# Optimization experiments

Hardware: AMD Instinct MI355X
Metric: run time of the kernel (lower is better)

The kernel has to match this reference:

```python
import jax, jax.numpy as jnp
import numpy as np
from jax import lax

K = 31      # avg_pool kernel
PAD = 15    # avg_pool padding (count_include_pad=True, torch default)
EPS = 1e-07

def _box_avg(x):
    # avg_pool2d(kernel=31, stride=1, padding=15), divisor includes zero padding
    s = lax.reduce_window(x, 0.0, lax.add, (1, 1, K, K), (1, 1, 1, 1),
                          [(0, 0), (0, 0), (PAD, PAD), (PAD, PAD)])
    return s / (K * K)

def _bce_logits(x, t):
    # stable elementwise BCE-with-logits
    return jnp.maximum(x, 0.0) - x * t + jnp.log1p(jnp.exp(-jnp.abs(x)))

def setup_inputs() -> dict:
    key = jax.random.key(0)
    k1, k2 = jax.random.split(key)
    B, C, H, W = 32, 1, 384, 384
    inp = jax.random.normal(k1, (B, C, H, W), dtype=jnp.float32)
    tgt = jax.random.uniform(k2, (B, C, H, W), dtype=jnp.float32)
    return {"input": inp, "target": tgt}

def reference(input, target):
    weit = 1.0 + 5.0 * jnp.abs(_box_avg(target) - target)          # [B,C,H,W]
    wbce = _bce_logits(input, target)                               # elementwise
    weit_sum = weit.sum(axis=(2, 3))                                # [B,C]
    wbce = (weit * wbce).sum(axis=(2, 3)) / weit_sum                # [B,C]
    p = jax.nn.sigmoid(input)
    inter = (p * target * weit).sum(axis=(2, 3))                    # [B,C]
    union = ((p + target) * weit).sum(axis=(2, 3))                  # [B,C]
    wiou = 1.0 - (inter + 1.0) / (union - inter + 1.0 + EPS)
    return (wbce + wiou).mean()
```

## Files before the change

kernel.cpp:

```cpp
#include <hip/hip_runtime.h>
#include <math.h>

#define NB   32
#define NH   384
#define NW   384
#define NPIX (NH * NW)
#define KRAD 15
#define KSZ  31
#define INV_DIV (1.0f / 961.0f)
#define EPSV 1e-7f

__global__ __launch_bounds__(256) void hbox_kernel(
    const float* __restrict__ tgt,
    float* __restrict__ hsum,
    float* __restrict__ accum)
{
    if (blockIdx.x == 0 && threadIdx.x < 128) accum[threadIdx.x] = 0.0f;

    const int PW = 16 + NW + 16;
    __shared__ float sp[4][16 + NW + 16];

    const int row0 = blockIdx.x * 4;
    const int tid  = threadIdx.x;

    if (tid < 128) {
        int r = tid >> 5, j = tid & 31;
        int col = (j < 16) ? j : (16 + NW + (j - 16));
        sp[r][col] = 0.0f;
    }
    for (int i = tid; i < 384; i += 256) {
        int r = i / 96, q = i % 96;
        float4 v = *reinterpret_cast<const float4*>(&tgt[(size_t)(row0 + r) * NW + q * 4]);
        *reinterpret_cast<float4*>(&sp[r][16 + q * 4]) = v;
    }
    __syncthreads();

    const int r  = tid >> 6;
    const int l  = tid & 63;
    const int x0 = l * 6;

    float res[6];
    float w = 0.0f;
    #pragma unroll
    for (int k = 0; k < KSZ; ++k) w += sp[r][x0 + 1 + k];
    res[0] = w;
    #pragma unroll
    for (int i = 1; i < 6; ++i) {
        w += sp[r][x0 + i + 31] - sp[r][x0 + i];
        res[i] = w;
    }
    __syncthreads();

    float* ob = &sp[0][0];
    #pragma unroll
    for (int i = 0; i < 6; ++i) ob[r * NW + x0 + i] = res[i];
    __syncthreads();
    for (int i = tid; i < 384; i += 256) {
        int rr = i / 96, q = i % 96;
        float4 v = *reinterpret_cast<float4*>(&ob[rr * NW + q * 4]);
        *reinterpret_cast<float4*>(&hsum[(size_t)(row0 + rr) * NW + q * 4]) = v;
    }
}

__global__ __launch_bounds__(384) void fused_kernel(
    const float* __restrict__ xin,
    const float* __restrict__ tgt,
    const float* __restrict__ hsum,
    float* __restrict__ accum)
{
    const int YTG = 6;
    const int b    = blockIdx.x >> 4;
    const int tile = blockIdx.x & 15;
    const int tid  = threadIdx.x;
    const int rg   = tid / 96;
    const int q    = tid % 96;
    const int c0   = q * 4;
    const int y0   = tile * 24 + rg * YTG;

    const float* __restrict__ hs = hsum + (size_t)b * NPIX;
    const float* __restrict__ tb = tgt  + (size_t)b * NPIX;
    const float* __restrict__ ib = xin  + (size_t)b * NPIX;

    float w0 = 0.0f, w1 = 0.0f, w2 = 0.0f, w3 = 0.0f;
    #pragma unroll
    for (int k = 0; k < KSZ; ++k) {
        int rr = y0 - KRAD + k;
        if (rr >= 0 && rr < NH) {
            float4 h = *reinterpret_cast<const float4*>(&hs[(size_t)rr * NW + c0]);
            w0 += h.x; w1 += h.y; w2 += h.z; w3 += h.w;
        }
    }

    float s_w = 0.0f, s_wb = 0.0f, s_i = 0.0f, s_u = 0.0f;

    #pragma unroll
    for (int yy = 0; yy < YTG; ++yy) {
        const int y = y0 + yy;
        float4 t4 = *reinterpret_cast<const float4*>(&tb[(size_t)y * NW + c0]);
        float4 v4 = *reinterpret_cast<const float4*>(&ib[(size_t)y * NW + c0]);

        const float wv[4] = {w0, w1, w2, w3};
        const float tv[4] = {t4.x, t4.y, t4.z, t4.w};
        const float vv[4] = {v4.x, v4.y, v4.z, v4.w};
        #pragma unroll
        for (int j = 0; j < 4; ++j) {
            const float bavg = wv[j] * INV_DIV;
            const float t = tv[j];
            const float v = vv[j];
            const float weit = 1.0f + 5.0f * fabsf(bavg - t);
            const float e    = expf(-fabsf(v));
            const float wbce = fmaxf(v, 0.0f) - v * t + log1pf(e);
            const float p    = (v >= 0.0f) ? 1.0f / (1.0f + e) : e / (1.0f + e);
            s_w  += weit;
            s_wb += weit * wbce;
            s_i  += p * t * weit;
            s_u  += (p + t) * weit;
        }

        const int add_r = y + KRAD + 1;
        const int sub_r = y - KRAD;
        if (add_r < NH) {
            float4 h = *reinterpret_cast<const float4*>(&hs[(size_t)add_r * NW + c0]);
            w0 += h.x; w1 += h.y; w2 += h.z; w3 += h.w;
        }
        if (sub_r >= 0) {
            float4 h = *reinterpret_cast<const float4*>(&hs[(size_t)sub_r * NW + c0]);
            w0 -= h.x; w1 -= h.y; w2 -= h.z; w3 -= h.w;
        }
    }

    #pragma unroll
    for (int off = 32; off > 0; off >>= 1) {
        s_w  += __shfl_down(s_w,  off);
        s_wb += __shfl_down(s_wb, off);
        s_i  += __shfl_down(s_i,  off);
        s_u  += __shfl_down(s_u,  off);
    }
    __shared__ float red[6][4];
    const int lane = tid & 63;
    const int wv_  = tid >> 6;
    if (lane == 0) {
        red[wv_][0] = s_w; red[wv_][1] = s_wb; red[wv_][2] = s_i; red[wv_][3] = s_u;
    }
    __syncthreads();
    if (tid < 4) {
        float acc = 0.0f;
        #pragma unroll
        for (int i = 0; i < 6; ++i) acc += red[i][tid];
        atomicAdd(&accum[b * 4 + tid], acc);
    }
}

__global__ __launch_bounds__(64) void finalize_kernel(
    const float* __restrict__ accum,
    float* __restrict__ out)
{
    __shared__ float ls[NB];
    const int t = threadIdx.x;
    if (t < NB) {
        const float sw  = accum[4 * t + 0];
        const float swb = accum[4 * t + 1];
        const float si  = accum[4 * t + 2];
        const float su  = accum[4 * t + 3];
        const float wbce = swb / sw;
        const float wiou = 1.0f - (si + 1.0f) / (su - si + 1.0f + EPSV);
        ls[t] = wbce + wiou;
    }
    __syncthreads();
    if (t == 0) {
        float s = 0.0f;
        #pragma unroll
        for (int i = 0; i < NB; ++i) s += ls[i];
        out[0] = s * (1.0f / (float)NB);
    }
}

extern "C" void kernel_launch(void* const* d_in, const int* in_sizes, int n_in,
                              void* d_out, int out_size, void* d_ws, size_t ws_size,
                              hipStream_t stream)
{
    const float* xin = (const float*)d_in[0];
    const float* tgt = (const float*)d_in[1];
    float* hsum  = (float*)d_ws;
    float* accum = hsum + (size_t)NB * NPIX;

    hbox_kernel    <<<(NB * NH) / 4, 256, 0, stream>>>(tgt, hsum, accum);
    fused_kernel   <<<NB * 16,       384, 0, stream>>>(xin, tgt, hsum, accum);
    finalize_kernel<<<1,             64,  0, stream>>>(accum, (float*)d_out);
}
```

Measured before the change: 121.2 us.

## Remap fused kernel to one column per thread with 12-row tiles

```diff
diff --git a/kernel.cpp b/kernel.cpp
--- a/kernel.cpp
+++ b/kernel.cpp
@@ -17,7 +17,6 @@
 {
     if (blockIdx.x == 0 && threadIdx.x < 128) accum[threadIdx.x] = 0.0f;
 
-    const int PW = 16 + NW + 16;
     __shared__ float sp[4][16 + NW + 16];
 
     const int row0 = blockIdx.x * 4;
@@ -62,70 +61,82 @@
     }
 }
 
-__global__ __launch_bounds__(384) void fused_kernel(
+__device__ __forceinline__ void loss_accum(float wsum, float t, float v,
+                                           float& s_w, float& s_wb,
+                                           float& s_i, float& s_u)
+{
+    const float bavg = wsum * INV_DIV;
+    const float weit = 1.0f + 5.0f * fabsf(bavg - t);
+    const float e    = expf(-fabsf(v));
+    const float wbce = fmaxf(v, 0.0f) - v * t + log1pf(e);
+    const float p    = (v >= 0.0f) ? 1.0f / (1.0f + e) : e / (1.0f + e);
+    s_w  += weit;
+    s_wb += weit * wbce;
+    s_i  += p * t * weit;
+    s_u  += (p + t) * weit;
+}
+
+__global__ __launch_bounds__(384, 8) void fused_kernel(
     const float* __restrict__ xin,
     const float* __restrict__ tgt,
     const float* __restrict__ hsum,
     float* __restrict__ accum)
 {
-    const int YTG = 6;
-    const int b    = blockIdx.x >> 4;
-    const int tile = blockIdx.x & 15;
-    const int tid  = threadIdx.x;
-    const int rg   = tid / 96;
-    const int q    = tid % 96;
-    const int c0   = q * 4;
-    const int y0   = tile * 24 + rg * YTG;
-
-    const float* __restrict__ hs = hsum + (size_t)b * NPIX;
-    const float* __restrict__ tb = tgt  + (size_t)b * NPIX;
-    const float* __restrict__ ib = xin  + (size_t)b * NPIX;
-
-    float w0 = 0.0f, w1 = 0.0f, w2 = 0.0f, w3 = 0.0f;
-    #pragma unroll
-    for (int k = 0; k < KSZ; ++k) {
-        int rr = y0 - KRAD + k;
-        if (rr >= 0 && rr < NH) {
-            float4 h = *reinterpret_cast<const float4*>(&hs[(size_t)rr * NW + c0]);
-            w0 += h.x; w1 += h.y; w2 += h.z; w3 += h.w;
-        }
-    }
+    const int blk  = blockIdx.x;
+    const int img  = ((blk & 7) << 2) | ((blk >> 3) & 3);
+    const int tile = blk >> 5;
+    const int x    = threadIdx.x;
+    const int y0   = tile * 12;
+
+    const float* __restrict__ hs = hsum + (size_t)img * NPIX + x;
+    const float* __restrict__ tb = tgt  + (size_t)img * NPIX + x;
+    const float* __restrict__ ib = xin  + (size_t)img * NPIX + x;
 
     float s_w = 0.0f, s_wb = 0.0f, s_i = 0.0f, s_u = 0.0f;
-
-    #pragma unroll
-    for (int yy = 0; yy < YTG; ++yy) {
-        const int y = y0 + yy;
-        float4 t4 = *reinterpret_cast<const float4*>(&tb[(size_t)y * NW + c0]);
-        float4 v4 = *reinterpret_cast<const float4*>(&ib[(size_t)y * NW + c0]);
-
-        const float wv[4] = {w0, w1, w2, w3};
-        const float tv[4] = {t4.x, t4.y, t4.z, t4.w};
-        const float vv[4] = {v4.x, v4.y, v4.z, v4.w};
-        #pragma unroll
-        for (int j = 0; j < 4; ++j) {
-            const float bavg = wv[j] * INV_DIV;
-            const float t = tv[j];
-            const float v = vv[j];
-            const float weit = 1.0f + 5.0f * fabsf(bavg - t);
-            const float e    = expf(-fabsf(v));
-            const float wbce = fmaxf(v, 0.0f) - v * t + log1pf(e);
-            const float p    = (v >= 0.0f) ? 1.0f / (1.0f + e) : e / (1.0f + e);
-            s_w  += weit;
-            s_wb += weit * wbce;
-            s_i  += p * t * weit;
-            s_u  += (p + t) * weit;
-        }
-
-        const int add_r = y + KRAD + 1;
-        const int sub_r = y - KRAD;
-        if (add_r < NH) {
-            float4 h = *reinterpret_cast<const float4*>(&hs[(size_t)add_r * NW + c0]);
-            w0 += h.x; w1 += h.y; w2 += h.z; w3 += h.w;
-        }
-        if (sub_r >= 0) {
-            float4 h = *reinterpret_cast<const float4*>(&hs[(size_t)sub_r * NW + c0]);
-            w0 -= h.x; w1 -= h.y; w2 -= h.z; w3 -= h.w;
+    float w;
+
+    const bool interior = (tile >= 2) && (tile <= 29);
+    if (interior) {
+        float wa = 0.0f, wb = 0.0f, wc = 0.0f, wd = 0.0f;
+        #pragma unroll
+        for (int k = 0; k < 28; k += 4) {
+            wa += hs[(y0 - KRAD + k + 0) * NW];
+            wb += hs[(y0 - KRAD + k + 1) * NW];
+            wc += hs[(y0 - KRAD + k + 2) * NW];
+            wd += hs[(y0 - KRAD + k + 3) * NW];
+        }
+        wa += hs[(y0 + 13) * NW];
+        wb += hs[(y0 + 14) * NW];
+        wc += hs[(y0 + 15) * NW];
+        w = (wa + wb) + (wc + wd);
+
+        #pragma unroll
+        for (int yy = 0; yy < 12; ++yy) {
+            const int y = y0 + yy;
+            const float t    = tb[y * NW];
+            const float v    = ib[y * NW];
+            const float hadd = hs[(y + KRAD + 1) * NW];
+            const float hsub = hs[(y - KRAD) * NW];
+            loss_accum(w, t, v, s_w, s_wb, s_i, s_u);
+            w += hadd - hsub;
+        }
+    } else {
+        w = 0.0f;
+        #pragma unroll
+        for (int k = 0; k < KSZ; ++k) {
+            const int rr = y0 - KRAD + k;
+            if (rr >= 0 && rr < NH) w += hs[rr * NW];
+        }
+        #pragma unroll
+        for (int yy = 0; yy < 12; ++yy) {
+            const int y = y0 + yy;
+            const float t = tb[y * NW];
+            const float v = ib[y * NW];
+            loss_accum(w, t, v, s_w, s_wb, s_i, s_u);
+            const int ra = y + KRAD + 1;
+            const int rs = y - KRAD;
+            if (ra < NH)  w += hs[ra * NW];
+            if (rs >= 0)  w -= hs[rs * NW];
         }
     }
 
@@ -137,17 +148,17 @@
         s_u  += __shfl_down(s_u,  off);
     }
     __shared__ float red[6][4];
-    const int lane = tid & 63;
-    const int wv_  = tid >> 6;
+    const int lane = threadIdx.x & 63;
+    const int wv   = threadIdx.x >> 6;
     if (lane == 0) {
-        red[wv_][0] = s_w; red[wv_][1] = s_wb; red[wv_][2] = s_i; red[wv_][3] = s_u;
-    }
-    __syncthreads();
-    if (tid < 4) {
+        red[wv][0] = s_w; red[wv][1] = s_wb; red[wv][2] = s_i; red[wv][3] = s_u;
+    }
+    __syncthreads();
+    if (threadIdx.x < 4) {
         float acc = 0.0f;
         #pragma unroll
-        for (int i = 0; i < 6; ++i) acc += red[i][tid];
-        atomicAdd(&accum[b * 4 + tid], acc);
+        for (int i = 0; i < 6; ++i) acc += red[i][threadIdx.x];
+        atomicAdd(&accum[img * 4 + threadIdx.x], acc);
     }
 }
 
@@ -185,6 +196,6 @@
     float* accum = hsum + (size_t)NB * NPIX;
 
     hbox_kernel    <<<(NB * NH) / 4, 256, 0, stream>>>(tgt, hsum, accum);
-    fused_kernel   <<<NB * 16,       384, 0, stream>>>(xin, tgt, hsum, accum);
+    fused_kernel   <<<NB * 32,       384, 0, stream>>>(xin, tgt, hsum, accum);
     finalize_kernel<<<1,             64,  0, stream>>>(accum, (float*)d_out);
 }
```

Result: faster. 114.5 us (-5.6%).

## Replace vertical sliding window with column prefix sums in separate kernel

Applied to the files above, without the earlier changes.

```diff
diff --git a/kernel.cpp b/kernel.cpp
--- a/kernel.cpp
+++ b/kernel.cpp
@@ -17,7 +17,6 @@
 {
     if (blockIdx.x == 0 && threadIdx.x < 128) accum[threadIdx.x] = 0.0f;
 
-    const int PW = 16 + NW + 16;
     __shared__ float sp[4][16 + NW + 16];
 
     const int row0 = blockIdx.x * 4;
@@ -62,70 +61,92 @@
     }
 }
 
-__global__ __launch_bounds__(384) void fused_kernel(
+__global__ __launch_bounds__(384) void vprefix_kernel(
+    const float* __restrict__ hsum,
+    float* __restrict__ P)
+{
+    const int b = blockIdx.x;
+    const int x = threadIdx.x;
+    const float* __restrict__ src = hsum + (size_t)b * NPIX + x;
+    float* __restrict__ dst       = P    + (size_t)b * NPIX + x;
+
+    float run = 0.0f;
+    for (int y = 0; y < NH; y += 16) {
+        float v[16];
+        #pragma unroll
+        for (int i = 0; i < 16; ++i) v[i] = src[(size_t)(y + i) * NW];
+        #pragma unroll
+        for (int i = 0; i < 16; ++i) {
+            run += v[i];
+            dst[(size_t)(y + i) * NW] = run;
+        }
+    }
+}
+
+__device__ __forceinline__ void loss_accum(float wsum, float t, float v,
+                                           float& s_w, float& s_wb,
+                                           float& s_i, float& s_u)
+{
+    const float bavg = wsum * INV_DIV;
+    const float weit = 1.0f + 5.0f * fabsf(bavg - t);
+    const float e    = expf(-fabsf(v));
+    const float wbce = fmaxf(v, 0.0f) - v * t + log1pf(e);
+    const float p    = (v >= 0.0f) ? 1.0f / (1.0f + e) : e / (1.0f + e);
+    s_w  += weit;
+    s_wb += weit * wbce;
+    s_i  += p * t * weit;
+    s_u  += (p + t) * weit;
+}
+
+__global__ __launch_bounds__(384, 4) void fused_kernel(
     const float* __restrict__ xin,
     const float* __restrict__ tgt,
-    const float* __restrict__ hsum,
+    const float* __restrict__ P,
     float* __restrict__ accum)
 {
-    const int YTG = 6;
-    const int b    = blockIdx.x >> 4;
-    const int tile = blockIdx.x & 15;
+    const int blk  = blockIdx.x;
+    const int img  = blk / 24;
+    const int tile = blk % 24;
     const int tid  = threadIdx.x;
+    const int q    = tid % 96;
     const int rg   = tid / 96;
-    const int q    = tid % 96;
     const int c0   = q * 4;
-    const int y0   = tile * 24 + rg * YTG;
-
-    const float* __restrict__ hs = hsum + (size_t)b * NPIX;
-    const float* __restrict__ tb = tgt  + (size_t)b * NPIX;
-    const float* __restrict__ ib = xin  + (size_t)b * NPIX;
-
-    float w0 = 0.0f, w1 = 0.0f, w2 = 0.0f, w3 = 0.0f;
-    #pragma unroll
-    for (int k = 0; k < KSZ; ++k) {
-        int rr = y0 - KRAD + k;
-        if (rr >= 0 && rr < NH) {
-            float4 h = *reinterpret_cast<const float4*>(&hs[(size_t)rr * NW + c0]);
-            w0 += h.x; w1 += h.y; w2 += h.z; w3 += h.w;
+    const int y0   = tile * 16 + rg * 4;
+
+    const float* __restrict__ Pb = P   + (size_t)img * NPIX;
+    const float* __restrict__ tb = tgt + (size_t)img * NPIX;
+    const float* __restrict__ ib = xin + (size_t)img * NPIX;
+
+    float s_w = 0.0f, s_wb = 0.0f, s_i = 0.0f, s_u = 0.0f;
+
+    if (tile >= 1 && tile <= 22) {
+        #pragma unroll
+        for (int i = 0; i < 4; ++i) {
+            const int y = y0 + i;
+            const float4 phi = *reinterpret_cast<const float4*>(&Pb[(size_t)(y + KRAD) * NW + c0]);
+            const float4 plo = *reinterpret_cast<const float4*>(&Pb[(size_t)(y - KRAD - 1) * NW + c0]);
+            const float4 t4  = *reinterpret_cast<const float4*>(&tb[(size_t)y * NW + c0]);
+            const float4 v4  = *reinterpret_cast<const float4*>(&ib[(size_t)y * NW + c0]);
+            loss_accum(phi.x - plo.x, t4.x, v4.x, s_w, s_wb, s_i, s_u);
+            loss_accum(phi.y - plo.y, t4.y, v4.y, s_w, s_wb, s_i, s_u);
+            loss_accum(phi.z - plo.z, t4.z, v4.z, s_w, s_wb, s_i, s_u);
+            loss_accum(phi.w - plo.w, t4.w, v4.w, s_w, s_wb, s_i, s_u);
         }
-    }
-
-    float s_w = 0.0f, s_wb = 0.0f, s_i = 0.0f, s_u = 0.0f;
-
-    #pragma unroll
-    for (int yy = 0; yy < YTG; ++yy) {
-        const int y = y0 + yy;
-        float4 t4 = *reinterpret_cast<const float4*>(&tb[(size_t)y * NW + c0]);
-        float4 v4 = *reinterpret_cast<const float4*>(&ib[(size_t)y * NW + c0]);
-
-        const float wv[4] = {w0, w1, w2, w3};
-        const float tv[4] = {t4.x, t4.y, t4.z, t4.w};
-        const float vv[4] = {v4.x, v4.y, v4.z, v4.w};
-        #pragma unroll
-        for (int j = 0; j < 4; ++j) {
-            const float bavg = wv[j] * INV_DIV;
-            const float t = tv[j];
-            const float v = vv[j];
-            const float weit = 1.0f + 5.0f * fabsf(bavg - t);
-            const float e    = expf(-fabsf(v));
-            const float wbce = fmaxf(v, 0.0f) - v * t + log1pf(e);
-            const float p    = (v >= 0.0f) ? 1.0f / (1.0f + e) : e / (1.0f + e);
-            s_w  += weit;
-            s_wb += weit * wbce;
-            s_i  += p * t * weit;
-            s_u  += (p + t) * weit;
-        }
-
-        const int add_r = y + KRAD + 1;
-        const int sub_r = y - KRAD;
-        if (add_r < NH) {
-            float4 h = *reinterpret_cast<const float4*>(&hs[(size_t)add_r * NW + c0]);
-            w0 += h.x; w1 += h.y; w2 += h.z; w3 += h.w;
-        }
-        if (sub_r >= 0) {
-            float4 h = *reinterpret_cast<const float4*>(&hs[(size_t)sub_r * NW + c0]);
-            w0 -= h.x; w1 -= h.y; w2 -= h.z; w3 -= h.w;
+    } else {
+        #pragma unroll
+        for (int i = 0; i < 4; ++i) {
+            const int y   = y0 + i;
+            const int yhi = (y + KRAD > NH - 1) ? (NH - 1) : (y + KRAD);
+            const float4 phi = *reinterpret_cast<const float4*>(&Pb[(size_t)yhi * NW + c0]);
+            float4 plo = make_float4(0.0f, 0.0f, 0.0f, 0.0f);
+            if (y >= KRAD + 1)
+                plo = *reinterpret_cast<const float4*>(&Pb[(size_t)(y - KRAD - 1) * NW + c0]);
+            const float4 t4 = *reinterpret_cast<const float4*>(&tb[(size_t)y * NW + c0]);
+            const float4 v4 = *reinterpret_cast<const float4*>(&ib[(size_t)y * NW + c0]);
+            loss_accum(phi.x - plo.x, t4.x, v4.x, s_w, s_wb, s_i, s_u);
+            loss_accum(phi.y - plo.y, t4.y, v4.y, s_w, s_wb, s_i, s_u);
+            loss_accum(phi.z - plo.z, t4.z, v4.z, s_w, s_wb, s_i, s_u);
+            loss_accum(phi.w - plo.w, t4.w, v4.w, s_w, s_wb, s_i, s_u);
         }
     }
 
@@ -138,16 +159,16 @@
     }
     __shared__ float red[6][4];
     const int lane = tid & 63;
-    const int wv_  = tid >> 6;
+    const int wv   = tid >> 6;
     if (lane == 0) {
-        red[wv_][0] = s_w; red[wv_][1] = s_wb; red[wv_][2] = s_i; red[wv_][3] = s_u;
+        red[wv][0] = s_w; red[wv][1] = s_wb; red[wv][2] = s_i; red[wv][3] = s_u;
     }
     __syncthreads();
     if (tid < 4) {
         float acc = 0.0f;
         #pragma unroll
         for (int i = 0; i < 6; ++i) acc += red[i][tid];
-        atomicAdd(&accum[b * 4 + tid], acc);
+        atomicAdd(&accum[img * 4 + tid], acc);
     }
 }
 
@@ -182,9 +203,11 @@
     const float* xin = (const float*)d_in[0];
     const float* tgt = (const float*)d_in[1];
     float* hsum  = (float*)d_ws;
-    float* accum = hsum + (size_t)NB * NPIX;
+    float* P     = hsum + (size_t)NB * NPIX;
+    float* accum = P + (size_t)NB * NPIX;
 
     hbox_kernel    <<<(NB * NH) / 4, 256, 0, stream>>>(tgt, hsum, accum);
-    fused_kernel   <<<NB * 16,       384, 0, stream>>>(xin, tgt, hsum, accum);
+    vprefix_kernel <<<NB,            384, 0, stream>>>(hsum, P);
+    fused_kernel   <<<NB * 24,       384, 0, stream>>>(xin, tgt, P, accum);
     finalize_kernel<<<1,             64,  0, stream>>>(accum, (float*)d_out);
 }
```

After: 124.1 us. 2.3% more time.
